# Performance work log

Hardware: AMD Instinct MI355X
Metric: run time of the kernel (lower is better)

## Reference

```python
import jax, jax.numpy as jnp
import numpy as np

H = 1024        # hidden_size
NH = 16         # num_heads
HD = H // NH    # head_dim
NS = 3          # num_strata


def setup_inputs() -> dict:
    key = jax.random.key(0)
    ks = jax.random.split(key, 12)
    s = 1.0 / np.sqrt(H)
    inp = {
        "hidden_states": jax.random.normal(ks[0], (2, 2048, H), dtype=jnp.float32),
        "Wq": jax.random.uniform(ks[1], (H, H), minval=-s, maxval=s, dtype=jnp.float32),
        "bq": jax.random.uniform(ks[2], (H,), minval=-s, maxval=s, dtype=jnp.float32),
        "Wk": jax.random.uniform(ks[3], (H, H), minval=-s, maxval=s, dtype=jnp.float32),
        "bk": jax.random.uniform(ks[4], (H,), minval=-s, maxval=s, dtype=jnp.float32),
        "Wv": jax.random.uniform(ks[5], (H, H), minval=-s, maxval=s, dtype=jnp.float32),
        "bv": jax.random.uniform(ks[6], (H,), minval=-s, maxval=s, dtype=jnp.float32),
        "Ws": jax.random.uniform(ks[7], (NS, H, H), minval=-s, maxval=s, dtype=jnp.float32),
        "bs": jax.random.uniform(ks[8], (NS, H), minval=-s, maxval=s, dtype=jnp.float32),
        "Wo": jax.random.uniform(ks[9], (H, H), minval=-s, maxval=s, dtype=jnp.float32),
        "bo": jax.random.uniform(ks[10], (H,), minval=-s, maxval=s, dtype=jnp.float32),
    }
    return inp


def reference(hidden_states, Wq, bq, Wk, bk, Wv, bv, Ws, bs, Wo, bo):
    B, S, _ = hidden_states.shape
    # torch nn.Linear: y = x @ W.T + b
    q = hidden_states @ Wq.T + bq
    k = hidden_states @ Wk.T + bk
    v = hidden_states @ Wv.T + bv
    # [B, NH, S, HD]
    q = q.reshape(B, S, NH, HD).transpose(0, 2, 1, 3)
    k = k.reshape(B, S, NH, HD).transpose(0, 2, 1, 3)
    v = v.reshape(B, S, NH, HD).transpose(0, 2, 1, 3)
    scores = jnp.einsum('bhqd,bhkd->bhqk', q, k) / jnp.sqrt(jnp.float32(HD))
    attn = jax.nn.softmax(scores, axis=-1)
    out = jnp.einsum('bhqk,bhkd->bhqd', attn, v)
    attn_output = out.transpose(0, 2, 1, 3).reshape(B, S, H)
    # stratum projections, averaged: [NS, B, S, H] -> mean over strata
    strata = jnp.einsum('bsh,ngh->nbsg', attn_output, Ws) + bs[:, None, None, :]
    enhanced = strata.mean(axis=0)
    output = enhanced @ Wo.T + bo
    return output
```

## Files before the change

kernel.cpp:

```cpp
#include <hip/hip_runtime.h>
#include <stdint.h>

typedef __attribute__((ext_vector_type(8))) short short8;
typedef __attribute__((ext_vector_type(4))) short short4v;
typedef __attribute__((ext_vector_type(4))) float f32x4;
typedef __attribute__((ext_vector_type(2))) unsigned int u32x2;
typedef unsigned int u32;
typedef const __attribute__((address_space(1))) u32* gas_ptr;
typedef __attribute__((address_space(3))) u32* las_ptr;

#define QSCALE 0.18033688011112042f

__device__ inline short f2bf(float x) {
    u32 u = __float_as_uint(x);
    u = u + 0x7FFFu + ((u >> 16) & 1u);
    return (short)(u >> 16);
}
__device__ inline void gload16(const void* g, void* l) {
    __builtin_amdgcn_global_load_lds((gas_ptr)g, (las_ptr)l, 16, 0, 0);
}

__global__ __launch_bounds__(256) void prep(const float* __restrict__ X,
                                            const float* __restrict__ Wq,
                                            const float* __restrict__ Wk,
                                            const float* __restrict__ Wv,
                                            const float* __restrict__ Wo,
                                            const float* __restrict__ Ws,
                                            const float* __restrict__ bs,
                                            const float* __restrict__ bo,
                                            short* __restrict__ Xb,
                                            short* __restrict__ Wcat,
                                            short* __restrict__ Wob,
                                            short* __restrict__ WmT,
                                            float* __restrict__ bc) {
    __shared__ short T[64][65];
    const int tid = threadIdx.x;
    const int bid = blockIdx.x;
    if (bid < 8192) {
        const float* src;
        short* dst;
        int rel;
        if (bid < 4096)      { src = X;  dst = Xb;                rel = bid; }
        else if (bid < 5120) { src = Wq; dst = Wcat;              rel = bid - 4096; }
        else if (bid < 6144) { src = Wk; dst = Wcat + (1 << 20);  rel = bid - 5120; }
        else if (bid < 7168) { src = Wv; dst = Wcat + (2 << 20);  rel = bid - 6144; }
        else                 { src = Wo; dst = Wob;               rel = bid - 7168; }
        int i = (rel * 256 + tid) * 4;
        float4 v = *(const float4*)&src[i];
        short4v o;
        o[0] = f2bf(v.x); o[1] = f2bf(v.y); o[2] = f2bf(v.z); o[3] = f2bf(v.w);
        *(short4v*)&dst[i] = o;
    } else if (bid < 8448) {
        const int id = bid - 8192;
        const int gx = (id & 15) * 64, jy = (id >> 4) * 64;
        const int HH = 1 << 20;
        for (int e = tid; e < 4096; e += 256) {
            int j = e >> 6, g = e & 63;
            int idx = (jy + j) * 1024 + gx + g;
            float v = (Ws[idx] + Ws[idx + HH] + Ws[idx + 2 * HH]) * (1.0f / 3.0f);
            T[g][j] = f2bf(v);
        }
        __syncthreads();
        for (int e = tid; e < 4096; e += 256) {
            int g = e >> 6, j = e & 63;
            WmT[(long)(gx + g) * 1024 + jy + j] = T[g][j];
        }
    } else {
        const int lane = tid & 63;
        const int n = (bid - 8448) * 4 + (tid >> 6);
        float acc = 0.0f;
        for (int j0 = 0; j0 < 1024; j0 += 64) {
            int j = j0 + lane;
            float bm = (bs[j] + bs[j + 1024] + bs[j + 2048]) * (1.0f / 3.0f);
            acc += Wo[(long)n * 1024 + j] * bm;
        }
#pragma unroll
        for (int off = 1; off < 64; off <<= 1) acc += __shfl_xor(acc, off, 64);
        if (lane == 0) bc[n] = acc + bo[n];
    }
}

__global__ __launch_bounds__(256) void gemm_qkvwc(const short* __restrict__ Xb,
                                                  const short* __restrict__ Wcat,
                                                  const short* __restrict__ Wob,
                                                  const short* __restrict__ WmT,
                                                  const float* __restrict__ bq,
                                                  const float* __restrict__ bk,
                                                  const float* __restrict__ bv,
                                                  short* __restrict__ Qb,
                                                  short* __restrict__ Kb,
                                                  short* __restrict__ Vt,
                                                  short* __restrict__ Wc) {
    __shared__ short As[128 * 64];
    __shared__ short Bs[128 * 64];
    const int K = 1024;
    const int tid  = threadIdx.x;
    const int lane = tid & 63;
    const int wave = tid >> 6;
    const int quad = lane >> 4;
    const int l16  = lane & 15;
    const int bid = blockIdx.x;
    const short *A, *W;
    int m0, n0, sel;
    if (bid < 768) {
        m0 = (bid & 31) * 128;
        int t = bid >> 5;
        sel = t >> 3;
        n0 = (t & 7) * 128;
        A = Xb;
        W = Wcat + (long)sel * (1 << 20);
    } else {
        int w = bid - 768;
        sel = 3;
        m0 = (w >> 3) * 128;
        n0 = (w & 7) * 128;
        A = Wob;
        W = WmT;
    }
    const int wm = (wave >> 1) * 64;
    const int wn = (wave & 1) * 64;

    f32x4 acc[4][4] = {};
    const int srow = tid >> 3, scol = (tid & 7) * 8;

    for (int k0 = 0; k0 < K; k0 += 64) {
#pragma unroll
        for (int i = 0; i < 4; i++) {
            gload16(&A[(long)(m0 + i * 32 + srow) * K + k0 + scol], &As[i * 2048 + wave * 512]);
            gload16(&W[(long)(n0 + i * 32 + srow) * K + k0 + scol], &Bs[i * 2048 + wave * 512]);
        }
        __syncthreads();
        short8 bfr[4][2];
#pragma unroll
        for (int ni = 0; ni < 4; ni++) {
            bfr[ni][0] = *(short8*)&Bs[(wn + ni * 16 + l16) * 64 + quad * 8];
            bfr[ni][1] = *(short8*)&Bs[(wn + ni * 16 + l16) * 64 + 32 + quad * 8];
        }
#pragma unroll
        for (int mi = 0; mi < 4; mi++) {
            short8 af0 = *(short8*)&As[(wm + mi * 16 + l16) * 64 + quad * 8];
            short8 af1 = *(short8*)&As[(wm + mi * 16 + l16) * 64 + 32 + quad * 8];
#pragma unroll
            for (int ni = 0; ni < 4; ni++) {
                acc[mi][ni] = __builtin_amdgcn_mfma_f32_16x16x32_bf16(af0, bfr[ni][0],
                                                                      acc[mi][ni], 0, 0, 0);
                acc[mi][ni] = __builtin_amdgcn_mfma_f32_16x16x32_bf16(af1, bfr[ni][1],
                                                                      acc[mi][ni], 0, 0, 0);
            }
        }
        __syncthreads();
    }

#pragma unroll
    for (int mi = 0; mi < 4; mi++) {
#pragma unroll
        for (int ni = 0; ni < 4; ni++) {
            const int n = n0 + wn + ni * 16 + l16;
            const int mbase = m0 + wm + mi * 16 + quad * 4;
            float bv2 = 0.0f;
            if (sel == 0) bv2 = bq[n];
            else if (sel == 1) bv2 = bk[n];
            else if (sel == 2) bv2 = bv[n];
            if (sel == 2) {
                short4v pk;
#pragma unroll
                for (int r = 0; r < 4; r++) pk[r] = f2bf(acc[mi][ni][r] + bv2);
                long addr = ((long)(mbase >> 11) << 21) + (long)n * 2048 + (mbase & 2047);
                *(short4v*)&Vt[addr] = pk;
            } else if (sel == 0) {
#pragma unroll
                for (int r = 0; r < 4; r++)
                    Qb[(long)(mbase + r) * 1024 + n] = f2bf((acc[mi][ni][r] + bv2) * QSCALE);
            } else {
                short* C = (sel == 1) ? Kb : Wc;
#pragma unroll
                for (int r = 0; r < 4; r++)
                    C[(long)(mbase + r) * 1024 + n] = f2bf(acc[mi][ni][r] + bv2);
            }
        }
    }
}

__global__ __launch_bounds__(256) void attn_kernel(const short* __restrict__ Q,
                                                   const short* __restrict__ Kb,
                                                   const short* __restrict__ Vt,
                                                   short* __restrict__ O) {
    __shared__ short Ks[64 * 72];
    __shared__ short Vs[64 * 72];
    __shared__ short Ps[4 * 16 * 72];
    const int tid  = threadIdx.x;
    const int lane = tid & 63;
    const int wave = tid >> 6;
    const int quad = lane >> 4;
    const int l16  = lane & 15;
    const int q0 = blockIdx.x * 64;
    const int h  = blockIdx.y;
    const int b  = blockIdx.z;

    short8 qf0, qf1;
    {
        long base = (long)(b * 2048 + q0 + wave * 16 + l16) * 1024 + h * 64 + quad * 8;
        qf0 = *(const short8*)&Q[base];
        qf1 = *(const short8*)&Q[base + 32];
    }

    const int sr0 = tid >> 3, sg0 = (tid & 7) * 8;
    const int sr1 = sr0 + 32;
    const short* Kp = Kb + (long)(b * 2048) * 1024 + h * 64;
    const short* Vp = Vt + ((long)b << 21) + (long)h * 64 * 2048;

    short8 pk0 = *(const short8*)&Kp[(long)sr0 * 1024 + sg0];
    short8 pk1 = *(const short8*)&Kp[(long)sr1 * 1024 + sg0];
    short8 pv0 = *(const short8*)&Vp[(long)sr0 * 2048 + sg0];
    short8 pv1 = *(const short8*)&Vp[(long)sr1 * 2048 + sg0];

    f32x4 o[4] = {};
    float lsum = 0.0f;

    u32* const pw = (u32*)&Ps[wave * 1152 + l16 * 72 + quad * 4];
    const short* const pr = &Ps[wave * 1152 + l16 * 72 + quad * 8];

    for (int kt = 0; kt < 32; kt++) {
        *(short8*)&Ks[sr0 * 72 + sg0] = pk0;
        *(short8*)&Ks[sr1 * 72 + sg0] = pk1;
        *(short8*)&Vs[sr0 * 72 + sg0] = pv0;
        *(short8*)&Vs[sr1 * 72 + sg0] = pv1;
        __syncthreads();

        {
            const int kbn = ((kt + 1) & 31) * 64;
            pk0 = *(const short8*)&Kp[(long)(kbn + sr0) * 1024 + sg0];
            pk1 = *(const short8*)&Kp[(long)(kbn + sr1) * 1024 + sg0];
            pv0 = *(const short8*)&Vp[(long)sr0 * 2048 + kbn + sg0];
            pv1 = *(const short8*)&Vp[(long)sr1 * 2048 + kbn + sg0];
        }

#pragma unroll
        for (int ni = 0; ni < 4; ni++) {
            short8 ak0 = *(short8*)&Ks[(ni * 16 + l16) * 72 + quad * 8];
            short8 ak1 = *(short8*)&Ks[(ni * 16 + l16) * 72 + 32 + quad * 8];
            f32x4 s = {};
            s = __builtin_amdgcn_mfma_f32_16x16x32_bf16(ak0, qf0, s, 0, 0, 0);
            s = __builtin_amdgcn_mfma_f32_16x16x32_bf16(ak1, qf1, s, 0, 0, 0);
            float p0 = __builtin_amdgcn_exp2f(s[0]);
            float p1 = __builtin_amdgcn_exp2f(s[1]);
            float p2 = __builtin_amdgcn_exp2f(s[2]);
            float p3 = __builtin_amdgcn_exp2f(s[3]);
            lsum += (p0 + p1) + (p2 + p3);
            u32 a0 = __float_as_uint(p0) + 0x8000u;
            u32 a1 = __float_as_uint(p1) + 0x8000u;
            u32 a2 = __float_as_uint(p2) + 0x8000u;
            u32 a3 = __float_as_uint(p3) + 0x8000u;
            u32x2 w;
            w[0] = __builtin_amdgcn_perm(a1, a0, 0x07060302u);
            w[1] = __builtin_amdgcn_perm(a3, a2, 0x07060302u);
            *(u32x2*)(pw + ni * 8) = w;
        }

        short8 ap0 = *(short8*)pr;
        short8 ap1 = *(short8*)(pr + 32);
#pragma unroll
        for (int ni = 0; ni < 4; ni++) {
            short8 bv0 = *(short8*)&Vs[(ni * 16 + l16) * 72 + quad * 8];
            short8 bv1 = *(short8*)&Vs[(ni * 16 + l16) * 72 + 32 + quad * 8];
            o[ni] = __builtin_amdgcn_mfma_f32_16x16x32_bf16(ap0, bv0, o[ni], 0, 0, 0);
            o[ni] = __builtin_amdgcn_mfma_f32_16x16x32_bf16(ap1, bv1, o[ni], 0, 0, 0);
        }
        __syncthreads();
    }

    lsum += __shfl_xor(lsum, 16, 64);
    lsum += __shfl_xor(lsum, 32, 64);
#pragma unroll
    for (int r = 0; r < 4; r++) {
        const float tot = __shfl(lsum, quad * 4 + r, 64);
        const float inv = 1.0f / tot;
        const long row = (long)(b * 2048 + q0 + wave * 16 + quad * 4 + r) * 1024 + h * 64;
#pragma unroll
        for (int ni = 0; ni < 4; ni++)
            O[row + ni * 16 + l16] = f2bf(o[ni][r] * inv);
    }
}

__global__ __launch_bounds__(256) void gemm_final(const short* __restrict__ A,
                                                  const short* __restrict__ W,
                                                  const float* __restrict__ bias,
                                                  float* __restrict__ C) {
    __shared__ short As[64 * 32];
    __shared__ short Bs[128 * 32];
    const int K = 1024;
    const int tid  = threadIdx.x;
    const int lane = tid & 63;
    const int wave = tid >> 6;
    const int quad = lane >> 4;
    const int l16  = lane & 15;
    const int bid = blockIdx.x;
    const int m0 = (bid >> 3) * 64;
    const int n0 = (bid & 7) * 128;
    const int wm = (wave >> 1) * 32;
    const int wn = (wave & 1) * 64;

    f32x4 acc[2][4] = {};
    const int r0 = tid >> 2, kk0 = (tid & 3) * 8;

    for (int k0 = 0; k0 < K; k0 += 32) {
        gload16(&A[(long)(m0 + r0) * K + k0 + kk0], &As[wave * 512]);
        gload16(&W[(long)(n0 + r0) * K + k0 + kk0], &Bs[wave * 512]);
        gload16(&W[(long)(n0 + r0 + 64) * K + k0 + kk0], &Bs[2048 + wave * 512]);
        __syncthreads();
        short8 af[2], bfr[4];
#pragma unroll
        for (int mi = 0; mi < 2; mi++)
            af[mi] = *(short8*)&As[(wm + mi * 16 + l16) * 32 + quad * 8];
#pragma unroll
        for (int ni = 0; ni < 4; ni++)
            bfr[ni] = *(short8*)&Bs[(wn + ni * 16 + l16) * 32 + quad * 8];
#pragma unroll
        for (int mi = 0; mi < 2; mi++)
#pragma unroll
            for (int ni = 0; ni < 4; ni++)
                acc[mi][ni] = __builtin_amdgcn_mfma_f32_16x16x32_bf16(af[mi], bfr[ni],
                                                                      acc[mi][ni], 0, 0, 0);
        __syncthreads();
    }

#pragma unroll
    for (int mi = 0; mi < 2; mi++) {
#pragma unroll
        for (int ni = 0; ni < 4; ni++) {
            const int n = n0 + wn + ni * 16 + l16;
            const float bv = bias[n];
            const int mbase = m0 + wm + mi * 16 + quad * 4;
#pragma unroll
            for (int r = 0; r < 4; r++)
                C[(long)(mbase + r) * 1024 + n] = acc[mi][ni][r] + bv;
        }
    }
}

extern "C" void kernel_launch(void* const* d_in, const int* in_sizes, int n_in,
                              void* d_out, int out_size, void* d_ws, size_t ws_size,
                              hipStream_t stream) {
    const float* X  = (const float*)d_in[0];
    const float* Wq = (const float*)d_in[1];
    const float* bq = (const float*)d_in[2];
    const float* Wk = (const float*)d_in[3];
    const float* bk = (const float*)d_in[4];
    const float* Wv = (const float*)d_in[5];
    const float* bv = (const float*)d_in[6];
    const float* Ws = (const float*)d_in[7];
    const float* bs = (const float*)d_in[8];
    const float* Wo = (const float*)d_in[9];
    const float* bo = (const float*)d_in[10];

    char* ws = (char*)d_ws;
    const long MB = 1 << 20;
    short* Xb   = (short*)(ws + 0 * MB);
    short* Wcat = (short*)(ws + 8 * MB);
    short* WmT  = (short*)(ws + 14 * MB);
    short* Wob  = (short*)(ws + 16 * MB);
    short* Wc   = (short*)(ws + 18 * MB);
    float* bc   = (float*)(ws + 20 * MB);
    short* Qb   = (short*)(ws + 21 * MB);
    short* Kbf  = (short*)(ws + 29 * MB);
    short* Vtb  = (short*)(ws + 37 * MB);
    short* AO   = Xb;

    dim3 bb(256);

    prep<<<dim3(8704), bb, 0, stream>>>(X, Wq, Wk, Wv, Wo, Ws, bs, bo,
                                        Xb, Wcat, Wob, WmT, bc);
    gemm_qkvwc<<<dim3(832), bb, 0, stream>>>(Xb, Wcat, Wob, WmT, bq, bk, bv,
                                             Qb, Kbf, Vtb, Wc);
    attn_kernel<<<dim3(32, 16, 2), bb, 0, stream>>>(Qb, Kbf, Vtb, AO);
    gemm_final<<<dim3(512), bb, 0, stream>>>(AO, Wc, bc, (float*)d_out);
}
```

Baseline: 243.8 us.

## XOR-swizzle LDS tiles and double-buffer attention K/V via direct global-to-LDS loads

Applies an XOR swizzle to the 16-byte chunks of the LDS tiles in the projection GEMM, the final GEMM and the attention kernel, so that MFMA fragment reads avoid bank conflicts without padding. The attention kernel now streams K/V tiles straight into a double-buffered LDS pair with global_load_lds, replacing register prefetch plus LDS stores, and drops one barrier per iteration. The final GEMM's K step grows from 32 to 64, halving the loop iterations and barriers. The cost is more LDS per block, which may reduce occupancy, plus more complex index arithmetic.

```diff
diff --git a/kernel.cpp b/kernel.cpp
--- a/kernel.cpp
+++ b/kernel.cpp
@@ -16,7 +16,7 @@
     u = u + 0x7FFFu + ((u >> 16) & 1u);
     return (short)(u >> 16);
 }
-__device__ inline void gload16(const void* g, void* l) {
+__device__ inline void gload16(const void* g, const void* l) {
     __builtin_amdgcn_global_load_lds((gas_ptr)g, (las_ptr)l, 16, 0, 0);
 }
 
@@ -121,25 +121,31 @@
     const int wn = (wave & 1) * 64;
 
     f32x4 acc[4][4] = {};
-    const int srow = tid >> 3, scol = (tid & 7) * 8;
+    const int sr = tid >> 3;
+    const int scol = (((tid & 7) ^ (sr & 7)) << 3);
+    const int fo_a = ((quad ^ (l16 & 7)) << 3);
+    const int fo_b = (((4 + quad) ^ (l16 & 7)) << 3);
 
     for (int k0 = 0; k0 < K; k0 += 64) {
 #pragma unroll
         for (int i = 0; i < 4; i++) {
-            gload16(&A[(long)(m0 + i * 32 + srow) * K + k0 + scol], &As[i * 2048 + wave * 512]);
-            gload16(&W[(long)(n0 + i * 32 + srow) * K + k0 + scol], &Bs[i * 2048 + wave * 512]);
+            int r = i * 32 + sr;
+            gload16(&A[(long)(m0 + r) * K + k0 + scol], &As[i * 2048 + wave * 512]);
+            gload16(&W[(long)(n0 + r) * K + k0 + scol], &Bs[i * 2048 + wave * 512]);
         }
         __syncthreads();
         short8 bfr[4][2];
 #pragma unroll
         for (int ni = 0; ni < 4; ni++) {
-            bfr[ni][0] = *(short8*)&Bs[(wn + ni * 16 + l16) * 64 + quad * 8];
-            bfr[ni][1] = *(short8*)&Bs[(wn + ni * 16 + l16) * 64 + 32 + quad * 8];
+            const int row = wn + ni * 16 + l16;
+            bfr[ni][0] = *(short8*)&Bs[row * 64 + fo_a];
+            bfr[ni][1] = *(short8*)&Bs[row * 64 + fo_b];
         }
 #pragma unroll
         for (int mi = 0; mi < 4; mi++) {
-            short8 af0 = *(short8*)&As[(wm + mi * 16 + l16) * 64 + quad * 8];
-            short8 af1 = *(short8*)&As[(wm + mi * 16 + l16) * 64 + 32 + quad * 8];
+            const int row = wm + mi * 16 + l16;
+            short8 af0 = *(short8*)&As[row * 64 + fo_a];
+            short8 af1 = *(short8*)&As[row * 64 + fo_b];
 #pragma unroll
             for (int ni = 0; ni < 4; ni++) {
                 acc[mi][ni] = __builtin_amdgcn_mfma_f32_16x16x32_bf16(af0, bfr[ni][0],
@@ -185,9 +191,9 @@
                                                    const short* __restrict__ Kb,
                                                    const short* __restrict__ Vt,
                                                    short* __restrict__ O) {
-    __shared__ short Ks[64 * 72];
-    __shared__ short Vs[64 * 72];
-    __shared__ short Ps[4 * 16 * 72];
+    __shared__ short Ks[2][64 * 64];
+    __shared__ short Vs[2][64 * 64];
+    __shared__ short Ps[4][16 * 64];
     const int tid  = threadIdx.x;
     const int lane = tid & 63;
     const int wave = tid >> 6;
@@ -204,41 +210,46 @@
         qf1 = *(const short8*)&Q[base + 32];
     }
 
-    const int sr0 = tid >> 3, sg0 = (tid & 7) * 8;
-    const int sr1 = sr0 + 32;
+    const int sr = tid >> 3;
+    const int scol = (((tid & 7) ^ (sr & 7)) << 3);
     const short* Kp = Kb + (long)(b * 2048) * 1024 + h * 64;
     const short* Vp = Vt + ((long)b << 21) + (long)h * 64 * 2048;
 
-    short8 pk0 = *(const short8*)&Kp[(long)sr0 * 1024 + sg0];
-    short8 pk1 = *(const short8*)&Kp[(long)sr1 * 1024 + sg0];
-    short8 pv0 = *(const short8*)&Vp[(long)sr0 * 2048 + sg0];
-    short8 pv1 = *(const short8*)&Vp[(long)sr1 * 2048 + sg0];
+    const int fo_a = ((quad ^ (l16 & 7)) << 3);
+    const int fo_b = (((4 + quad) ^ (l16 & 7)) << 3);
+    int po[4];
+#pragma unroll
+    for (int ni = 0; ni < 4; ni++)
+        po[ni] = l16 * 64 + ((((2 * ni) + (quad >> 1)) ^ (l16 & 7)) << 3) + ((quad & 1) << 2);
 
     f32x4 o[4] = {};
     float lsum = 0.0f;
 
-    u32* const pw = (u32*)&Ps[wave * 1152 + l16 * 72 + quad * 4];
-    const short* const pr = &Ps[wave * 1152 + l16 * 72 + quad * 8];
+#pragma unroll
+    for (int i = 0; i < 2; i++) {
+        int r = i * 32 + sr;
+        gload16(&Kp[(long)r * 1024 + scol], &Ks[0][i * 2048 + wave * 512]);
+        gload16(&Vp[(long)r * 2048 + scol], &Vs[0][i * 2048 + wave * 512]);
+    }
+    __syncthreads();
 
     for (int kt = 0; kt < 32; kt++) {
-        *(short8*)&Ks[sr0 * 72 + sg0] = pk0;
-        *(short8*)&Ks[sr1 * 72 + sg0] = pk1;
-        *(short8*)&Vs[sr0 * 72 + sg0] = pv0;
-        *(short8*)&Vs[sr1 * 72 + sg0] = pv1;
-        __syncthreads();
-
-        {
-            const int kbn = ((kt + 1) & 31) * 64;
-            pk0 = *(const short8*)&Kp[(long)(kbn + sr0) * 1024 + sg0];
-            pk1 = *(const short8*)&Kp[(long)(kbn + sr1) * 1024 + sg0];
-            pv0 = *(const short8*)&Vp[(long)sr0 * 2048 + kbn + sg0];
-            pv1 = *(const short8*)&Vp[(long)sr1 * 2048 + kbn + sg0];
-        }
-
-#pragma unroll
-        for (int ni = 0; ni < 4; ni++) {
-            short8 ak0 = *(short8*)&Ks[(ni * 16 + l16) * 72 + quad * 8];
-            short8 ak1 = *(short8*)&Ks[(ni * 16 + l16) * 72 + 32 + quad * 8];
+        const int cur = kt & 1;
+        if (kt < 31) {
+            const int kbn = (kt + 1) * 64;
+#pragma unroll
+            for (int i = 0; i < 2; i++) {
+                int r = i * 32 + sr;
+                gload16(&Kp[(long)(kbn + r) * 1024 + scol], &Ks[cur ^ 1][i * 2048 + wave * 512]);
+                gload16(&Vp[(long)r * 2048 + kbn + scol], &Vs[cur ^ 1][i * 2048 + wave * 512]);
+            }
+        }
+
+#pragma unroll
+        for (int ni = 0; ni < 4; ni++) {
+            const int row = ni * 16 + l16;
+            short8 ak0 = *(short8*)&Ks[cur][row * 64 + fo_a];
+            short8 ak1 = *(short8*)&Ks[cur][row * 64 + fo_b];
             f32x4 s = {};
             s = __builtin_amdgcn_mfma_f32_16x16x32_bf16(ak0, qf0, s, 0, 0, 0);
             s = __builtin_amdgcn_mfma_f32_16x16x32_bf16(ak1, qf1, s, 0, 0, 0);
@@ -254,15 +265,16 @@
             u32x2 w;
             w[0] = __builtin_amdgcn_perm(a1, a0, 0x07060302u);
             w[1] = __builtin_amdgcn_perm(a3, a2, 0x07060302u);
-            *(u32x2*)(pw + ni * 8) = w;
-        }
-
-        short8 ap0 = *(short8*)pr;
-        short8 ap1 = *(short8*)(pr + 32);
-#pragma unroll
-        for (int ni = 0; ni < 4; ni++) {
-            short8 bv0 = *(short8*)&Vs[(ni * 16 + l16) * 72 + quad * 8];
-            short8 bv1 = *(short8*)&Vs[(ni * 16 + l16) * 72 + 32 + quad * 8];
+            *(u32x2*)&Ps[wave][po[ni]] = w;
+        }
+
+        short8 ap0 = *(short8*)&Ps[wave][l16 * 64 + fo_a];
+        short8 ap1 = *(short8*)&Ps[wave][l16 * 64 + fo_b];
+#pragma unroll
+        for (int ni = 0; ni < 4; ni++) {
+            const int row = ni * 16 + l16;
+            short8 bv0 = *(short8*)&Vs[cur][row * 64 + fo_a];
+            short8 bv1 = *(short8*)&Vs[cur][row * 64 + fo_b];
             o[ni] = __builtin_amdgcn_mfma_f32_16x16x32_bf16(ap0, bv0, o[ni], 0, 0, 0);
             o[ni] = __builtin_amdgcn_mfma_f32_16x16x32_bf16(ap1, bv1, o[ni], 0, 0, 0);
         }
@@ -286,8 +298,8 @@
                                                   const short* __restrict__ W,
                                                   const float* __restrict__ bias,
                                                   float* __restrict__ C) {
-    __shared__ short As[64 * 32];
-    __shared__ short Bs[128 * 32];
+    __shared__ short As[64 * 64];
+    __shared__ short Bs[128 * 64];
     const int K = 1024;
     const int tid  = threadIdx.x;
     const int lane = tid & 63;
@@ -301,26 +313,43 @@
     const int wn = (wave & 1) * 64;
 
     f32x4 acc[2][4] = {};
-    const int r0 = tid >> 2, kk0 = (tid & 3) * 8;
-
-    for (int k0 = 0; k0 < K; k0 += 32) {
-        gload16(&A[(long)(m0 + r0) * K + k0 + kk0], &As[wave * 512]);
-        gload16(&W[(long)(n0 + r0) * K + k0 + kk0], &Bs[wave * 512]);
-        gload16(&W[(long)(n0 + r0 + 64) * K + k0 + kk0], &Bs[2048 + wave * 512]);
-        __syncthreads();
-        short8 af[2], bfr[4];
-#pragma unroll
-        for (int mi = 0; mi < 2; mi++)
-            af[mi] = *(short8*)&As[(wm + mi * 16 + l16) * 32 + quad * 8];
-#pragma unroll
-        for (int ni = 0; ni < 4; ni++)
-            bfr[ni] = *(short8*)&Bs[(wn + ni * 16 + l16) * 32 + quad * 8];
-#pragma unroll
-        for (int mi = 0; mi < 2; mi++)
-#pragma unroll
-            for (int ni = 0; ni < 4; ni++)
-                acc[mi][ni] = __builtin_amdgcn_mfma_f32_16x16x32_bf16(af[mi], bfr[ni],
+    const int sr = tid >> 3;
+    const int scol = (((tid & 7) ^ (sr & 7)) << 3);
+    const int fo_a = ((quad ^ (l16 & 7)) << 3);
+    const int fo_b = (((4 + quad) ^ (l16 & 7)) << 3);
+
+    for (int k0 = 0; k0 < K; k0 += 64) {
+#pragma unroll
+        for (int i = 0; i < 2; i++) {
+            int r = i * 32 + sr;
+            gload16(&A[(long)(m0 + r) * K + k0 + scol], &As[i * 2048 + wave * 512]);
+        }
+#pragma unroll
+        for (int i = 0; i < 4; i++) {
+            int r = i * 32 + sr;
+            gload16(&W[(long)(n0 + r) * K + k0 + scol], &Bs[i * 2048 + wave * 512]);
+        }
+        __syncthreads();
+        short8 bfr[4][2];
+#pragma unroll
+        for (int ni = 0; ni < 4; ni++) {
+            const int row = wn + ni * 16 + l16;
+            bfr[ni][0] = *(short8*)&Bs[row * 64 + fo_a];
+            bfr[ni][1] = *(short8*)&Bs[row * 64 + fo_b];
+        }
+#pragma unroll
+        for (int mi = 0; mi < 2; mi++) {
+            const int row = wm + mi * 16 + l16;
+            short8 af0 = *(short8*)&As[row * 64 + fo_a];
+            short8 af1 = *(short8*)&As[row * 64 + fo_b];
+#pragma unroll
+            for (int ni = 0; ni < 4; ni++) {
+                acc[mi][ni] = __builtin_amdgcn_mfma_f32_16x16x32_bf16(af0, bfr[ni][0],
                                                                       acc[mi][ni], 0, 0, 0);
+                acc[mi][ni] = __builtin_amdgcn_mfma_f32_16x16x32_bf16(af1, bfr[ni][1],
+                                                                      acc[mi][ni], 0, 0, 0);
+            }
+        }
         __syncthreads();
     }
 
```

After: 231.4 us. 1.05x faster.
